# Performance work log

Hardware: AMD Instinct MI355X
Metric: run time of the kernel (lower is better)

## Reference

```python
import jax, jax.numpy as jnp
import numpy as np

N_NODES = 100000
EPS = 1e-12


def _sage_conv(x, src, dst, Wl, bl, Wr):
    # PyG SAGEConv (aggr='mean'): lin_l(mean of neighbor msgs) + lin_r(x)
    msgs = x[src]                                                # [E, d] gather
    agg = jax.ops.segment_sum(msgs, dst, num_segments=N_NODES)  # [N, d] scatter-add
    deg = jax.ops.segment_sum(jnp.ones((src.shape[0],), x.dtype), dst,
                              num_segments=N_NODES)             # [N]
    agg = agg / jnp.maximum(deg, 1.0)[:, None]                  # scatter-mean
    return agg @ Wl + bl + x @ Wr


def setup_inputs() -> dict:
    key = jax.random.key(0)
    ks = jax.random.split(key, 16)
    d_in, d_h = 64, 64
    E = 1600000
    s = 0.1
    inp = {
        'x': jax.random.normal(ks[0], (N_NODES, d_in), jnp.float32),
        'edge_index': jax.random.randint(ks[1], (2, E), 0, N_NODES, jnp.int64),
    }
    dims = [(d_in, d_h), (d_h, d_h), (d_h, d_h), (d_h, d_h)]
    for i, (di, do) in enumerate(dims, start=1):
        inp[f'Wl{i}'] = s * jax.random.normal(ks[3 * i - 1], (di, do), jnp.float32)
        inp[f'bl{i}'] = jnp.zeros((do,), jnp.float32)
        inp[f'Wr{i}'] = s * jax.random.normal(ks[3 * i], (di, do), jnp.float32)
    return inp


def reference(x, edge_index, Wl1, bl1, Wr1, Wl2, bl2, Wr2, Wl3, bl3, Wr3, Wl4, bl4, Wr4):
    src, dst = edge_index[0], edge_index[1]
    # dropout is identity in eval mode
    h1 = jax.nn.relu(_sage_conv(x, src, dst, Wl1, bl1, Wr1))
    h2 = jax.nn.relu(_sage_conv(h1, src, dst, Wl2, bl2, Wr2)) + h1
    h3 = jax.nn.relu(_sage_conv(h2, src, dst, Wl3, bl3, Wr3)) + h2
    out = _sage_conv(h3, src, dst, Wl4, bl4, Wr4)
    # F.normalize(p=2, dim=1, eps=1e-12)
    norm = jnp.maximum(jnp.linalg.norm(out, axis=1, keepdims=True), EPS)
    return out / norm
```

## Files before the change

kernel.cpp:

```cpp
#include <hip/hip_runtime.h>


#include <hip/hip_bf16.h>

static inline size_t al256(size_t x) { return (x + 255) & ~(size_t)255; }

#define EPB 4096
#define CAP 16384

typedef _Float16 f16x8 __attribute__((ext_vector_type(8)));
typedef _Float16 h2v __attribute__((ext_vector_type(2)));
typedef float f32x4 __attribute__((ext_vector_type(4)));
typedef float f32x2 __attribute__((ext_vector_type(2)));
union HU { unsigned u32; h2v h; };
union Q4 { uint2 u; _Float16 hh[4]; };

#if defined(__has_builtin)
#if __has_builtin(__builtin_amdgcn_cvt_pk_f32_fp8) && __has_builtin(__builtin_amdgcn_cvt_pk_fp8_f32)
#define FP8_HW 1
#endif
#endif

__device__ inline unsigned char f32_to_fp8(float v) {
#ifdef FP8_HW
  int pk = __builtin_amdgcn_cvt_pk_fp8_f32(v, v, 0, false);
  return (unsigned char)(pk & 0xff);
#else
  union { _Float16 f; unsigned short u; } cv;
  cv.f = (_Float16)v;
  unsigned short h = cv.u;
  unsigned s = (h >> 15) & 1u;
  unsigned e = (h >> 10) & 0x1fu;
  unsigned m = h & 0x3ffu;
  if (e < 9u) return (unsigned char)(s << 7);
  unsigned keep = m >> 7;
  unsigned rnd = (m >> 6) & 1u;
  unsigned sticky = (m & 0x3fu) ? 1u : 0u;
  unsigned inc = rnd & (sticky | (keep & 1u));
  unsigned body = (((e - 8u) << 3) | keep) + inc;
  if (body > 0x7eu) body = 0x7eu;
  return (unsigned char)((s << 7) | body);
#endif
}

#ifndef FP8_HW
__device__ inline float fp8_to_f32(unsigned b) {
  unsigned m7 = b & 0x7fu;
  union { unsigned short u; _Float16 f; } cv;
  cv.u = (unsigned short)(((b & 0x80u) << 8) | (m7 ? ((m7 << 7) + 0x2000u) : 0u));
  return (float)cv.f;
}
#endif

__device__ inline void fp8x4_acc(unsigned u, float& s0, float& s1, float& s2, float& s3) {
#ifdef FP8_HW
  f32x2 lo = __builtin_amdgcn_cvt_pk_f32_fp8((int)u, false);
  f32x2 hi = __builtin_amdgcn_cvt_pk_f32_fp8((int)u, true);
  s0 += lo[0]; s1 += lo[1]; s2 += hi[0]; s3 += hi[1];
#else
  s0 += fp8_to_f32(u & 0xffu);
  s1 += fp8_to_f32((u >> 8) & 0xffu);
  s2 += fp8_to_f32((u >> 16) & 0xffu);
  s3 += fp8_to_f32(u >> 24);
#endif
}

__device__ inline int blk_detect(const unsigned int* __restrict__ raw, int E, int base) {
  __shared__ int fsh;
  int t = threadIdx.x;
  if (t == 0) fsh = 0;
  __syncthreads();
  if (t < 64) {
    int i = base + t;
    unsigned nz = (i < E) ? raw[2 * (size_t)i + 1] : 0u;
    unsigned long long b = __ballot(nz != 0u);
    if (t == 0 && b) fsh = 1;
  }
  __syncthreads();
  return fsh;
}

__global__ __launch_bounds__(256) void k_bscatter(const unsigned int* __restrict__ raw, int E,
                                                  int span, int* __restrict__ cursorB,
                                                  unsigned* __restrict__ bdata) {
  __shared__ int lh[256], lcur[256], gbase[256];
  int t = threadIdx.x;
  int base = blockIdx.x * EPB;
  int f = blk_detect(raw, E, base);
  lh[t] = 0;
  lcur[t] = 0;
  __syncthreads();
#pragma unroll 4
  for (int k = 0; k < EPB / 256; ++k) {
    int i = base + k * 256 + t;
    if (i < E) {
      int dst = f ? (int)raw[E + i] : (int)raw[2 * (size_t)(E + i)];
      atomicAdd(&lh[dst / span], 1);
    }
  }
  __syncthreads();
  int c = lh[t];
  gbase[t] = t * CAP + (c ? atomicAdd(&cursorB[t], c) : 0);
  __syncthreads();
#pragma unroll 4
  for (int k = 0; k < EPB / 256; ++k) {
    int i = base + k * 256 + t;
    if (i < E) {
      int s_, d_;
      if (f) { s_ = (int)raw[i]; d_ = (int)raw[E + i]; }
      else   { s_ = (int)raw[2 * (size_t)i]; d_ = (int)raw[2 * (size_t)(E + i)]; }
      int b = d_ / span;
      int pos = atomicAdd(&lcur[b], 1);
      bdata[(size_t)gbase[b] + pos] = ((unsigned)(d_ - b * span) << 17) | (unsigned)s_;
    }
  }
}

__global__ __launch_bounds__(256) void k_bbuild(const unsigned* __restrict__ bdata,
                                                const int* __restrict__ cursorB, int span, int N,
                                                int* __restrict__ csr, int2* __restrict__ begdeg) {
  __shared__ int cnt[512], sa[512], sb[512], cur[512];
  int b = blockIdx.x;
  int t = threadIdx.x;
  int node0 = b * span;
  int beg = b * CAP;
  int end = beg + cursorB[b];
  cnt[t] = 0;
  cnt[t + 256] = 0;
  __syncthreads();
  for (int i = beg + t; i < end; i += 256) {
    atomicAdd(&cnt[bdata[i] >> 17], 1);
  }
  __syncthreads();
  sa[t] = cnt[t];
  sa[t + 256] = cnt[t + 256];
  __syncthreads();
  int* s = sa;
  int* d = sb;
  for (int off = 1; off < 512; off <<= 1) {
    d[t] = s[t] + (t >= off ? s[t - off] : 0);
    int i2 = t + 256;
    d[i2] = s[i2] + (i2 >= off ? s[i2 - off] : 0);
    __syncthreads();
    int* tmp = s; s = d; d = tmp;
  }
  int ex0 = s[t] - cnt[t];
  int ex1 = s[t + 256] - cnt[t + 256];
  cur[t] = ex0;
  cur[t + 256] = ex1;
  if (t < span) {
    int node = node0 + t;
    if (node < N) begdeg[node] = make_int2(beg + ex0, cnt[t]);
  }
  int t2 = t + 256;
  if (t2 < span) {
    int node = node0 + t2;
    if (node < N) begdeg[node] = make_int2(beg + ex1, cnt[t2]);
  }
  __syncthreads();
  for (int i = beg + t; i < end; i += 256) {
    unsigned p = bdata[i];
    int pos = atomicAdd(&cur[p >> 17], 1);
    csr[beg + pos] = (int)(p & 0x1FFFFu);
  }
}

template <int IT, int P8>
__global__ __launch_bounds__(256) void k_gemm(
    const void* __restrict__ hv_, const float* __restrict__ Wl,
    const float* __restrict__ Wr, const float* __restrict__ bl,
    void* __restrict__ Pv, unsigned short* __restrict__ R16, int n) {
  __shared__ uint4 hAu[512];
  char* hAraw = (char*)hAu;
  int t = threadIdx.x;
  int n0 = blockIdx.x * 64;
  int w = t >> 6;
  int l = t & 63;
  int lo16 = l & 15;
  int g = l >> 4;

#pragma unroll
  for (int c = 0; c < 4; ++c) {
    int idx = t + c * 256;
    int row = idx >> 4;
    int fc = idx & 15;
    int nn = n0 + row;
    uint2 u = make_uint2(0u, 0u);
    if (nn < n) {
      if (IT == 0) {
        const float* h = (const float*)hv_;
        float4 hv = *(const float4*)&h[(size_t)nn * 64 + fc * 4];
        union { _Float16 p[4]; uint2 u; } cv;
        cv.p[0] = (_Float16)hv.x; cv.p[1] = (_Float16)hv.y;
        cv.p[2] = (_Float16)hv.z; cv.p[3] = (_Float16)hv.w;
        u = cv.u;
      } else {
        u = *(const uint2*)((const char*)hv_ + (size_t)nn * 128 + fc * 8);
      }
    }
    int byte = (row * 128 + fc * 8) ^ ((row & 7) << 4);
    *(uint2*)(hAraw + byte) = u;
  }

  const float* Wsel = (w < 2) ? Wl : Wr;
  int colbase = (w & 1) * 32;
  f16x8 bfr[2][2];
#pragma unroll
  for (int nf = 0; nf < 2; ++nf) {
    int j = colbase + nf * 16 + lo16;
#pragma unroll
    for (int kk = 0; kk < 2; ++kk) {
      int k0 = kk * 32 + g * 8;
      f16x8 bb;
#pragma unroll
      for (int s = 0; s < 8; ++s) bb[s] = (_Float16)Wsel[(k0 + s) * 64 + j];
      bfr[nf][kk] = bb;
    }
  }
  __syncthreads();

  f32x4 acc[4][2];
#pragma unroll
  for (int mf = 0; mf < 4; ++mf)
#pragma unroll
    for (int nf = 0; nf < 2; ++nf) acc[mf][nf] = (f32x4){0.f, 0.f, 0.f, 0.f};

#pragma unroll
  for (int mf = 0; mf < 4; ++mf) {
    int row = mf * 16 + lo16;
    int swz = (row & 7) << 4;
    f16x8 av0 = *(const f16x8*)(hAraw + row * 128 + ((g * 16) ^ swz));
    f16x8 av1 = *(const f16x8*)(hAraw + row * 128 + ((64 + g * 16) ^ swz));
#pragma unroll
    for (int nf = 0; nf < 2; ++nf) {
      acc[mf][nf] = __builtin_amdgcn_mfma_f32_16x16x32_f16(av0, bfr[nf][0], acc[mf][nf], 0, 0, 0);
      acc[mf][nf] = __builtin_amdgcn_mfma_f32_16x16x32_f16(av1, bfr[nf][1], acc[mf][nf], 0, 0, 0);
    }
  }

#pragma unroll
  for (int nf = 0; nf < 2; ++nf) {
    int col = colbase + nf * 16 + lo16;
    float bv = (w >= 2) ? bl[col] : 0.f;
#pragma unroll
    for (int mf = 0; mf < 4; ++mf) {
#pragma unroll
      for (int r = 0; r < 4; ++r) {
        int grow = n0 + mf * 16 + g * 4 + r;
        if (grow < n) {
          float v = acc[mf][nf][r];
          if (w < 2) {
            if (P8) {
              ((unsigned char*)Pv)[(size_t)grow * 64 + col] = f32_to_fp8(v);
            } else {
              union { _Float16 hh; unsigned short us; } cv;
              cv.hh = (_Float16)v;
              ((unsigned short*)Pv)[(size_t)grow * 64 + col] = cv.us;
            }
          } else {
            union { _Float16 hh; unsigned short us; } cv;
            cv.hh = (_Float16)(v + bv);
            R16[(size_t)grow * 64 + col] = cv.us;
          }
        }
      }
    }
  }
}

template <int MODE, int P8>
__global__ __launch_bounds__(256) void k_gatherP(
    const void* __restrict__ Pv, const unsigned short* __restrict__ R16,
    const unsigned short* __restrict__ hres, const int* __restrict__ csr,
    const int2* __restrict__ begdeg, void* __restrict__ hout, int n, int limit) {
  int t = threadIdx.x;
  int w = t >> 6;
  int l = t & 63;
  int half = l >> 5;
  int q = l & 15;
  int g2 = (l >> 4) & 1;
  int v = blockIdx.x * 8 + w * 2 + half;
  int bH = 0, rH = 0;
  if (v < n) {
    int2 bd = begdeg[v];
    bH = bd.x;
    rH = bd.y;
  }
  float idg = 1.0f / fmaxf((float)rH, 1.0f);
  Q4 rq; rq.u = make_uint2(0u, 0u);
  Q4 hq; hq.u = make_uint2(0u, 0u);
  if ((l & 16) == 0 && v < n) {
    rq.u = *(const uint2*)((const char*)R16 + (size_t)v * 128 + q * 8);
    if (MODE == 1) hq.u = *(const uint2*)((const char*)hres + (size_t)v * 128 + q * 8);
  }
  float s0 = 0.f, s1 = 0.f, s2 = 0.f, s3 = 0.f;
  int rOther = __shfl_xor(rH, 32, 64);
  int maxR = rH > rOther ? rH : rOther;
  int nb = (maxR + 15) >> 4;
  for (int bt = 0; bt < nb; ++bt) {
    int rem = rH - (bt << 4);
    int offc = (rem > 0) ? ((q < rem) ? q : rem - 1) : 0;
    int addr = bH + (bt << 4) + offc;
    addr = (addr < limit) ? addr : limit - 1;
    int myidx = csr[addr];
    myidx = (rem > 0) ? myidx : 0;
    int remMax = maxR - (bt << 4);
    if (P8) {
#pragma unroll
      for (int tt = 0; tt < 8; ++tt) {
        if (2 * tt >= remMax) break;
        int ee = 2 * tt + g2;
        int sel = __shfl(myidx, (half << 5) + ee, 64);
        unsigned u = ((const unsigned*)Pv)[(unsigned)((sel << 4) + q)];
        u = (ee < rem) ? u : 0u;
        fp8x4_acc(u, s0, s1, s2, s3);
      }
    } else {
      h2v a0 = (h2v)0, a1 = (h2v)0;
#pragma unroll
      for (int tt = 0; tt < 8; ++tt) {
        if (2 * tt >= remMax) break;
        int ee = 2 * tt + g2;
        int sel = __shfl(myidx, (half << 5) + ee, 64);
        uint2 u = ((const uint2*)Pv)[(unsigned)((sel << 4) + q)];
        bool m = ee < rem;
        HU b0, b1;
        b0.u32 = m ? u.x : 0u;
        b1.u32 = m ? u.y : 0u;
        a0 += b0.h;
        a1 += b1.h;
      }
      s0 += (float)a0[0];
      s1 += (float)a0[1];
      s2 += (float)a1[0];
      s3 += (float)a1[1];
    }
  }
  s0 += __shfl_xor(s0, 16, 64);
  s1 += __shfl_xor(s1, 16, 64);
  s2 += __shfl_xor(s2, 16, 64);
  s3 += __shfl_xor(s3, 16, 64);

  if ((l & 16) == 0 && v < n) {
    float4 o;
    o.x = s0 * idg + (float)rq.hh[0];
    o.y = s1 * idg + (float)rq.hh[1];
    o.z = s2 * idg + (float)rq.hh[2];
    o.w = s3 * idg + (float)rq.hh[3];
    if (MODE == 0) {
      o.x = fmaxf(o.x, 0.f); o.y = fmaxf(o.y, 0.f);
      o.z = fmaxf(o.z, 0.f); o.w = fmaxf(o.w, 0.f);
    } else if (MODE == 1) {
      o.x = fmaxf(o.x, 0.f) + (float)hq.hh[0];
      o.y = fmaxf(o.y, 0.f) + (float)hq.hh[1];
      o.z = fmaxf(o.z, 0.f) + (float)hq.hh[2];
      o.w = fmaxf(o.w, 0.f) + (float)hq.hh[3];
    } else {
      float sq = o.x * o.x + o.y * o.y + o.z * o.z + o.w * o.w;
#pragma unroll
      for (int m = 1; m < 16; m <<= 1) sq += __shfl_xor(sq, m, 64);
      float nrm = fmaxf(sqrtf(sq), 1e-12f);
      o.x /= nrm; o.y /= nrm; o.z /= nrm; o.w /= nrm;
    }
    if (MODE == 2) {
      *(float4*)&((float*)hout)[((size_t)v << 6) + (q << 2)] = o;
    } else {
      Q4 oq;
      oq.hh[0] = (_Float16)o.x; oq.hh[1] = (_Float16)o.y;
      oq.hh[2] = (_Float16)o.z; oq.hh[3] = (_Float16)o.w;
      *(uint2*)((char*)hout + (size_t)v * 128 + q * 8) = oq.u;
    }
  }
}

extern "C" void kernel_launch(void* const* d_in, const int* in_sizes, int n_in,
                              void* d_out, int out_size, void* d_ws, size_t ws_size,
                              hipStream_t stream) {
  const float* x = (const float*)d_in[0];
  const unsigned int* eraw = (const unsigned int*)d_in[1];
  const float* Wl[4] = {(const float*)d_in[2], (const float*)d_in[5],
                        (const float*)d_in[8], (const float*)d_in[11]};
  const float* blv[4] = {(const float*)d_in[3], (const float*)d_in[6],
                         (const float*)d_in[9], (const float*)d_in[12]};
  const float* Wr[4] = {(const float*)d_in[4], (const float*)d_in[7],
                        (const float*)d_in[10], (const float*)d_in[13]};
  const int N = in_sizes[0] / 64;
  const int E = in_sizes[1] / 2;
  const int span = (N + 255) / 256;
  const int limit = 256 * CAP;
  float* out = (float*)d_out;

  char* w = (char*)d_ws;
  size_t off = 0;
  int* cursorB = (int*)(w + off);     off = al256(off + 256 * 4);
  int* csr = (int*)(w + off);         off = al256(off + (size_t)256 * CAP * 4);
  unsigned* bdata = (unsigned*)(w + off); off = al256(off + (size_t)256 * CAP * 4);
  int2* begdeg = (int2*)(w + off);    off = al256(off + (size_t)N * 8);
  unsigned short* hA = (unsigned short*)(w + off); off = al256(off + (size_t)N * 64 * 2);
  unsigned short* hB = (unsigned short*)(w + off); off = al256(off + (size_t)N * 64 * 2);
  unsigned char* Pf8 = (unsigned char*)(w + off);  off = al256(off + (size_t)N * 64);
  unsigned short* Pf16 = (unsigned short*)(w + off); off = al256(off + (size_t)N * 64 * 2);
  unsigned short* R16 = (unsigned short*)(w + off); off = al256(off + (size_t)N * 64 * 2);

  hipMemsetAsync(cursorB, 0, 256 * 4, stream);

  int eb = (E + EPB - 1) / EPB;
  k_bscatter<<<eb, 256, 0, stream>>>(eraw, E, span, cursorB, bdata);
  k_bbuild<<<256, 256, 0, stream>>>(bdata, cursorB, span, N, csr, begdeg);

  int gb = (N + 63) / 64;
  int nb8 = (N + 7) / 8;
  k_gemm<0, 1><<<gb, 256, 0, stream>>>(x, Wl[0], Wr[0], blv[0], Pf8, R16, N);
  k_gatherP<0, 1><<<nb8, 256, 0, stream>>>(Pf8, R16, nullptr, csr, begdeg, hA, N, limit);
  k_gemm<1, 1><<<gb, 256, 0, stream>>>(hA, Wl[1], Wr[1], blv[1], Pf8, R16, N);
  k_gatherP<1, 1><<<nb8, 256, 0, stream>>>(Pf8, R16, hA, csr, begdeg, hB, N, limit);
  k_gemm<1, 0><<<gb, 256, 0, stream>>>(hB, Wl[2], Wr[2], blv[2], Pf16, R16, N);
  k_gatherP<1, 0><<<nb8, 256, 0, stream>>>(Pf16, R16, hB, csr, begdeg, hA, N, limit);
  k_gemm<1, 0><<<gb, 256, 0, stream>>>(hA, Wl[3], Wr[3], blv[3], Pf16, R16, N);
  k_gatherP<2, 0><<<nb8, 256, 0, stream>>>(Pf16, R16, nullptr, csr, begdeg, out, N, limit);
}
```

Measured before the change: 291.4 us.

## Slice feature tables into 8-dim column slabs and gather per slab

Stores P, R and hidden features in a sliced layout (8 slices of 8 fp16 dims per node) and replaces the per-node gather with a kernel where each block handles one slice for 128 nodes, so each neighbour fetch reads 16 bytes from a smaller, more cache-resident table. The fp8 path for early layers is dropped in favour of fp16 everywhere, and L2 normalisation moves to a separate final kernel. The aim is better L2 locality for random neighbour gathers, at the cost of eight times more csr reads, serial per-node loops with wave-wide shuffle reductions, fp16 accumulation, and an extra launch.

New measurement: 818.9 us. 2.81x slower.

```diff
diff --git a/kernel.cpp b/kernel.cpp
--- a/kernel.cpp
+++ b/kernel.cpp
@@ -11,59 +11,7 @@
 typedef _Float16 f16x8 __attribute__((ext_vector_type(8)));
 typedef _Float16 h2v __attribute__((ext_vector_type(2)));
 typedef float f32x4 __attribute__((ext_vector_type(4)));
-typedef float f32x2 __attribute__((ext_vector_type(2)));
 union HU { unsigned u32; h2v h; };
-union Q4 { uint2 u; _Float16 hh[4]; };
-
-#if defined(__has_builtin)
-#if __has_builtin(__builtin_amdgcn_cvt_pk_f32_fp8) && __has_builtin(__builtin_amdgcn_cvt_pk_fp8_f32)
-#define FP8_HW 1
-#endif
-#endif
-
-__device__ inline unsigned char f32_to_fp8(float v) {
-#ifdef FP8_HW
-  int pk = __builtin_amdgcn_cvt_pk_fp8_f32(v, v, 0, false);
-  return (unsigned char)(pk & 0xff);
-#else
-  union { _Float16 f; unsigned short u; } cv;
-  cv.f = (_Float16)v;
-  unsigned short h = cv.u;
-  unsigned s = (h >> 15) & 1u;
-  unsigned e = (h >> 10) & 0x1fu;
-  unsigned m = h & 0x3ffu;
-  if (e < 9u) return (unsigned char)(s << 7);
-  unsigned keep = m >> 7;
-  unsigned rnd = (m >> 6) & 1u;
-  unsigned sticky = (m & 0x3fu) ? 1u : 0u;
-  unsigned inc = rnd & (sticky | (keep & 1u));
-  unsigned body = (((e - 8u) << 3) | keep) + inc;
-  if (body > 0x7eu) body = 0x7eu;
-  return (unsigned char)((s << 7) | body);
-#endif
-}
-
-#ifndef FP8_HW
-__device__ inline float fp8_to_f32(unsigned b) {
-  unsigned m7 = b & 0x7fu;
-  union { unsigned short u; _Float16 f; } cv;
-  cv.u = (unsigned short)(((b & 0x80u) << 8) | (m7 ? ((m7 << 7) + 0x2000u) : 0u));
-  return (float)cv.f;
-}
-#endif
-
-__device__ inline void fp8x4_acc(unsigned u, float& s0, float& s1, float& s2, float& s3) {
-#ifdef FP8_HW
-  f32x2 lo = __builtin_amdgcn_cvt_pk_f32_fp8((int)u, false);
-  f32x2 hi = __builtin_amdgcn_cvt_pk_f32_fp8((int)u, true);
-  s0 += lo[0]; s1 += lo[1]; s2 += hi[0]; s3 += hi[1];
-#else
-  s0 += fp8_to_f32(u & 0xffu);
-  s1 += fp8_to_f32((u >> 8) & 0xffu);
-  s2 += fp8_to_f32((u >> 16) & 0xffu);
-  s3 += fp8_to_f32(u >> 24);
-#endif
-}
 
 __device__ inline int blk_detect(const unsigned int* __restrict__ raw, int E, int base) {
   __shared__ int fsh;
@@ -165,11 +113,11 @@
   }
 }
 
-template <int IT, int P8>
+template <int IT>
 __global__ __launch_bounds__(256) void k_gemm(
     const void* __restrict__ hv_, const float* __restrict__ Wl,
     const float* __restrict__ Wr, const float* __restrict__ bl,
-    void* __restrict__ Pv, unsigned short* __restrict__ R16, int n) {
+    unsigned short* __restrict__ Ps, unsigned short* __restrict__ Rs, int n) {
   __shared__ uint4 hAu[512];
   char* hAraw = (char*)hAu;
   int t = threadIdx.x;
@@ -182,23 +130,32 @@
 #pragma unroll
   for (int c = 0; c < 4; ++c) {
     int idx = t + c * 256;
-    int row = idx >> 4;
-    int fc = idx & 15;
-    int nn = n0 + row;
     uint2 u = make_uint2(0u, 0u);
-    if (nn < n) {
-      if (IT == 0) {
+    int row, dimb;
+    if (IT == 0) {
+      row = idx >> 4;
+      int fc = idx & 15;
+      dimb = fc * 8;
+      int nn = n0 + row;
+      if (nn < n) {
         const float* h = (const float*)hv_;
         float4 hv = *(const float4*)&h[(size_t)nn * 64 + fc * 4];
         union { _Float16 p[4]; uint2 u; } cv;
         cv.p[0] = (_Float16)hv.x; cv.p[1] = (_Float16)hv.y;
         cv.p[2] = (_Float16)hv.z; cv.p[3] = (_Float16)hv.w;
         u = cv.u;
-      } else {
-        u = *(const uint2*)((const char*)hv_ + (size_t)nn * 128 + fc * 8);
       }
-    }
-    int byte = (row * 128 + fc * 8) ^ ((row & 7) << 4);
+    } else {
+      int s = idx >> 7;
+      int r2 = idx & 127;
+      row = r2 >> 1;
+      int half = r2 & 1;
+      dimb = s * 16 + half * 8;
+      int nn = n0 + row;
+      if (nn < n)
+        u = *(const uint2*)((const char*)hv_ + ((size_t)s * n + nn) * 16 + half * 8);
+    }
+    int byte = (row * 128 + dimb) ^ ((row & 7) << 4);
     *(uint2*)(hAraw + byte) = u;
   }
 
@@ -242,6 +199,7 @@
   for (int nf = 0; nf < 2; ++nf) {
     int col = colbase + nf * 16 + lo16;
     float bv = (w >= 2) ? bl[col] : 0.f;
+    size_t sbase = ((size_t)(col >> 3) * n) * 8 + (col & 7);
 #pragma unroll
     for (int mf = 0; mf < 4; ++mf) {
 #pragma unroll
@@ -249,18 +207,13 @@
         int grow = n0 + mf * 16 + g * 4 + r;
         if (grow < n) {
           float v = acc[mf][nf][r];
+          union { _Float16 hh; unsigned short us; } cv;
           if (w < 2) {
-            if (P8) {
-              ((unsigned char*)Pv)[(size_t)grow * 64 + col] = f32_to_fp8(v);
-            } else {
-              union { _Float16 hh; unsigned short us; } cv;
-              cv.hh = (_Float16)v;
-              ((unsigned short*)Pv)[(size_t)grow * 64 + col] = cv.us;
-            }
+            cv.hh = (_Float16)v;
+            Ps[sbase + (size_t)grow * 8] = cv.us;
           } else {
-            union { _Float16 hh; unsigned short us; } cv;
             cv.hh = (_Float16)(v + bv);
-            R16[(size_t)grow * 64 + col] = cv.us;
+            Rs[sbase + (size_t)grow * 8] = cv.us;
           }
         }
       }
@@ -268,109 +221,85 @@
   }
 }
 
-template <int MODE, int P8>
-__global__ __launch_bounds__(256) void k_gatherP(
-    const void* __restrict__ Pv, const unsigned short* __restrict__ R16,
-    const unsigned short* __restrict__ hres, const int* __restrict__ csr,
-    const int2* __restrict__ begdeg, void* __restrict__ hout, int n, int limit) {
+template <int MODE>
+__global__ __launch_bounds__(256) void k_gatherS(
+    const unsigned* __restrict__ Ps, const unsigned* __restrict__ Rs,
+    const unsigned* __restrict__ hresS, const int* __restrict__ csr,
+    const int2* __restrict__ begdeg, void* __restrict__ hout, int n) {
   int t = threadIdx.x;
   int w = t >> 6;
   int l = t & 63;
-  int half = l >> 5;
-  int q = l & 15;
-  int g2 = (l >> 4) & 1;
-  int v = blockIdx.x * 8 + w * 2 + half;
-  int bH = 0, rH = 0;
-  if (v < n) {
+  int S = blockIdx.x & 7;
+  int chunk = blockIdx.x >> 3;
+  int es = l >> 2;
+  int d2 = l & 3;
+  unsigned sbase = (unsigned)S * (unsigned)n;
+  int vbase = chunk * 128 + w * 32;
+
+  for (int i = 0; i < 32; ++i) {
+    int v = vbase + i;
+    if (v >= n) break;
     int2 bd = begdeg[v];
-    bH = bd.x;
-    rH = bd.y;
-  }
-  float idg = 1.0f / fmaxf((float)rH, 1.0f);
-  Q4 rq; rq.u = make_uint2(0u, 0u);
-  Q4 hq; hq.u = make_uint2(0u, 0u);
-  if ((l & 16) == 0 && v < n) {
-    rq.u = *(const uint2*)((const char*)R16 + (size_t)v * 128 + q * 8);
-    if (MODE == 1) hq.u = *(const uint2*)((const char*)hres + (size_t)v * 128 + q * 8);
-  }
-  float s0 = 0.f, s1 = 0.f, s2 = 0.f, s3 = 0.f;
-  int rOther = __shfl_xor(rH, 32, 64);
-  int maxR = rH > rOther ? rH : rOther;
-  int nb = (maxR + 15) >> 4;
-  for (int bt = 0; bt < nb; ++bt) {
-    int rem = rH - (bt << 4);
-    int offc = (rem > 0) ? ((q < rem) ? q : rem - 1) : 0;
-    int addr = bH + (bt << 4) + offc;
-    addr = (addr < limit) ? addr : limit - 1;
-    int myidx = csr[addr];
-    myidx = (rem > 0) ? myidx : 0;
-    int remMax = maxR - (bt << 4);
-    if (P8) {
-#pragma unroll
-      for (int tt = 0; tt < 8; ++tt) {
-        if (2 * tt >= remMax) break;
-        int ee = 2 * tt + g2;
-        int sel = __shfl(myidx, (half << 5) + ee, 64);
-        unsigned u = ((const unsigned*)Pv)[(unsigned)((sel << 4) + q)];
-        u = (ee < rem) ? u : 0u;
-        fp8x4_acc(u, s0, s1, s2, s3);
+    int beg = bd.x, deg = bd.y;
+    h2v a = (h2v)0;
+    int nb = (deg + 15) >> 4;
+    for (int bt = 0; bt < nb; ++bt) {
+      int rem = deg - (bt << 4);
+      int offc = es < rem ? es : rem - 1;
+      int idx = csr[beg + (bt << 4) + offc];
+      unsigned u = Ps[(sbase + (unsigned)idx) * 4u + (unsigned)d2];
+      u = (es < rem) ? u : 0u;
+      HU b;
+      b.u32 = u;
+      a += b.h;
+    }
+    HU au;
+    au.h = a;
+#pragma unroll
+    for (int m = 4; m < 64; m <<= 1) {
+      HU o;
+      o.u32 = __shfl_xor(au.u32, m, 64);
+      au.h = au.h + o.h;
+    }
+    if (l < 4) {
+      float idg = 1.0f / fmaxf((float)deg, 1.0f);
+      float o0 = (float)au.h[0] * idg;
+      float o1 = (float)au.h[1] * idg;
+      HU r;
+      r.u32 = Rs[(sbase + (unsigned)v) * 4u + (unsigned)d2];
+      o0 += (float)r.h[0];
+      o1 += (float)r.h[1];
+      if (MODE == 2) {
+        *(float2*)&((float*)hout)[(size_t)v * 64 + S * 8 + d2 * 2] = make_float2(o0, o1);
+      } else {
+        o0 = fmaxf(o0, 0.f);
+        o1 = fmaxf(o1, 0.f);
+        if (MODE == 1) {
+          HU hr;
+          hr.u32 = hresS[(sbase + (unsigned)v) * 4u + (unsigned)d2];
+          o0 += (float)hr.h[0];
+          o1 += (float)hr.h[1];
+        }
+        HU ov;
+        ov.h[0] = (_Float16)o0;
+        ov.h[1] = (_Float16)o1;
+        ((unsigned*)hout)[(sbase + (unsigned)v) * 4u + (unsigned)d2] = ov.u32;
       }
-    } else {
-      h2v a0 = (h2v)0, a1 = (h2v)0;
-#pragma unroll
-      for (int tt = 0; tt < 8; ++tt) {
-        if (2 * tt >= remMax) break;
-        int ee = 2 * tt + g2;
-        int sel = __shfl(myidx, (half << 5) + ee, 64);
-        uint2 u = ((const uint2*)Pv)[(unsigned)((sel << 4) + q)];
-        bool m = ee < rem;
-        HU b0, b1;
-        b0.u32 = m ? u.x : 0u;
-        b1.u32 = m ? u.y : 0u;
-        a0 += b0.h;
-        a1 += b1.h;
-      }
-      s0 += (float)a0[0];
-      s1 += (float)a0[1];
-      s2 += (float)a1[0];
-      s3 += (float)a1[1];
-    }
-  }
-  s0 += __shfl_xor(s0, 16, 64);
-  s1 += __shfl_xor(s1, 16, 64);
-  s2 += __shfl_xor(s2, 16, 64);
-  s3 += __shfl_xor(s3, 16, 64);
-
-  if ((l & 16) == 0 && v < n) {
-    float4 o;
-    o.x = s0 * idg + (float)rq.hh[0];
-    o.y = s1 * idg + (float)rq.hh[1];
-    o.z = s2 * idg + (float)rq.hh[2];
-    o.w = s3 * idg + (float)rq.hh[3];
-    if (MODE == 0) {
-      o.x = fmaxf(o.x, 0.f); o.y = fmaxf(o.y, 0.f);
-      o.z = fmaxf(o.z, 0.f); o.w = fmaxf(o.w, 0.f);
-    } else if (MODE == 1) {
-      o.x = fmaxf(o.x, 0.f) + (float)hq.hh[0];
-      o.y = fmaxf(o.y, 0.f) + (float)hq.hh[1];
-      o.z = fmaxf(o.z, 0.f) + (float)hq.hh[2];
-      o.w = fmaxf(o.w, 0.f) + (float)hq.hh[3];
-    } else {
-      float sq = o.x * o.x + o.y * o.y + o.z * o.z + o.w * o.w;
-#pragma unroll
-      for (int m = 1; m < 16; m <<= 1) sq += __shfl_xor(sq, m, 64);
-      float nrm = fmaxf(sqrtf(sq), 1e-12f);
-      o.x /= nrm; o.y /= nrm; o.z /= nrm; o.w /= nrm;
-    }
-    if (MODE == 2) {
-      *(float4*)&((float*)hout)[((size_t)v << 6) + (q << 2)] = o;
-    } else {
-      Q4 oq;
-      oq.hh[0] = (_Float16)o.x; oq.hh[1] = (_Float16)o.y;
-      oq.hh[2] = (_Float16)o.z; oq.hh[3] = (_Float16)o.w;
-      *(uint2*)((char*)hout + (size_t)v * 128 + q * 8) = oq.u;
-    }
-  }
+    }
+  }
+}
+
+__global__ __launch_bounds__(256) void k_norm(float* __restrict__ o, int n) {
+  int w = threadIdx.x >> 6;
+  int l = threadIdx.x & 63;
+  int v = blockIdx.x * 4 + w;
+  if (v >= n) return;
+  float x = o[(size_t)v * 64 + l];
+  float sq = x * x;
+#pragma unroll
+  for (int m = 1; m < 64; m <<= 1) sq += __shfl_xor(sq, m, 64);
+  float nrm = fmaxf(sqrtf(sq), 1e-12f);
+  o[(size_t)v * 64 + l] = x / nrm;
 }
 
 extern "C" void kernel_launch(void* const* d_in, const int* in_sizes, int n_in,
@@ -387,7 +316,6 @@
   const int N = in_sizes[0] / 64;
   const int E = in_sizes[1] / 2;
   const int span = (N + 255) / 256;
-  const int limit = 256 * CAP;
   float* out = (float*)d_out;
 
   char* w = (char*)d_ws;
@@ -398,9 +326,8 @@
   int2* begdeg = (int2*)(w + off);    off = al256(off + (size_t)N * 8);
   unsigned short* hA = (unsigned short*)(w + off); off = al256(off + (size_t)N * 64 * 2);
   unsigned short* hB = (unsigned short*)(w + off); off = al256(off + (size_t)N * 64 * 2);
-  unsigned char* Pf8 = (unsigned char*)(w + off);  off = al256(off + (size_t)N * 64);
-  unsigned short* Pf16 = (unsigned short*)(w + off); off = al256(off + (size_t)N * 64 * 2);
-  unsigned short* R16 = (unsigned short*)(w + off); off = al256(off + (size_t)N * 64 * 2);
+  unsigned short* Ps = (unsigned short*)(w + off); off = al256(off + (size_t)N * 64 * 2);
+  unsigned short* Rs = (unsigned short*)(w + off); off = al256(off + (size_t)N * 64 * 2);
 
   hipMemsetAsync(cursorB, 0, 256 * 4, stream);
 
@@ -409,13 +336,17 @@
   k_bbuild<<<256, 256, 0, stream>>>(bdata, cursorB, span, N, csr, begdeg);
 
   int gb = (N + 63) / 64;
-  int nb8 = (N + 7) / 8;
-  k_gemm<0, 1><<<gb, 256, 0, stream>>>(x, Wl[0], Wr[0], blv[0], Pf8, R16, N);
-  k_gatherP<0, 1><<<nb8, 256, 0, stream>>>(Pf8, R16, nullptr, csr, begdeg, hA, N, limit);
-  k_gemm<1, 1><<<gb, 256, 0, stream>>>(hA, Wl[1], Wr[1], blv[1], Pf8, R16, N);
-  k_gatherP<1, 1><<<nb8, 256, 0, stream>>>(Pf8, R16, hA, csr, begdeg, hB, N, limit);
-  k_gemm<1, 0><<<gb, 256, 0, stream>>>(hB, Wl[2], Wr[2], blv[2], Pf16, R16, N);
-  k_gatherP<1, 0><<<nb8, 256, 0, stream>>>(Pf16, R16, hB, csr, begdeg, hA, N, limit);
-  k_gemm<1, 0><<<gb, 256, 0, stream>>>(hA, Wl[3], Wr[3], blv[3], Pf16, R16, N);
-  k_gatherP<2, 0><<<nb8, 256, 0, stream>>>(Pf16, R16, nullptr, csr, begdeg, out, N, limit);
-}
+  int gb8 = 8 * ((N + 127) / 128);
+  int nbn = (N + 3) / 4;
+  const unsigned* P1 = (const unsigned*)Ps;
+  const unsigned* R1 = (const unsigned*)Rs;
+  k_gemm<0><<<gb, 256, 0, stream>>>(x, Wl[0], Wr[0], blv[0], Ps, Rs, N);
+  k_gatherS<0><<<gb8, 256, 0, stream>>>(P1, R1, nullptr, csr, begdeg, hA, N);
+  k_gemm<1><<<gb, 256, 0, stream>>>(hA, Wl[1], Wr[1], blv[1], Ps, Rs, N);
+  k_gatherS<1><<<gb8, 256, 0, stream>>>(P1, R1, (const unsigned*)hA, csr, begdeg, hB, N);
+  k_gemm<1><<<gb, 256, 0, stream>>>(hB, Wl[2], Wr[2], blv[2], Ps, Rs, N);
+  k_gatherS<1><<<gb8, 256, 0, stream>>>(P1, R1, (const unsigned*)hB, csr, begdeg, hA, N);
+  k_gemm<1><<<gb, 256, 0, stream>>>(hA, Wl[3], Wr[3], blv[3], Ps, Rs, N);
+  k_gatherS<2><<<gb8, 256, 0, stream>>>(P1, R1, nullptr, csr, begdeg, out, N);
+  k_norm<<<nbn, 256, 0, stream>>>(out, N);
+}
```
